# Kernel tuning notes

Measured on AMD Instinct MI355X. Metric: run time of the kernel, lower is better.

## Reference

```python
import jax, jax.numpy as jnp
import numpy as np

SIZE = 14          # feature-map side (448 image / stride 32)
IMG_STRIDE = 32    # feature->image coordinate stride
RATIOS = [(4, 4), (3, 5), (5, 3), (6, 6), (5, 7), (7, 5), (8, 8), (6, 10), (10, 6)]
GROUPS = [(0, 3), (3, 6), (6, 9)]   # ratio index ranges per scale group
N_LIST = [3, 2, 1]                   # proposals kept per group (sum = proposalN = 6)
IOU_THRESHS = [0.25, 0.25, 0.25]
WIN_NUMS = [(SIZE - h + 1) * (SIZE - w + 1) for h, w in RATIOS]  # 121,120,120,81,80,80,49,45,45
OFFS = np.cumsum([0] + WIN_NUMS)


def _make_coords():
    # image-space [x0,y0,x1,y1] per window, same order as flattened avgpool outputs
    coords = []
    for h, w in RATIOS:
        Ho, Wo = SIZE - h + 1, SIZE - w + 1
        for i in range(Ho):
            for j in range(Wo):
                x0 = i * IMG_STRIDE - 1
                y0 = j * IMG_STRIDE - 1
                x1 = x0 + h * IMG_STRIDE
                y1 = y0 + w * IMG_STRIDE
                coords.append([max(x0, 0), max(y0, 0), x1, y1])
    return np.asarray(coords, np.int32)  # [741, 4]


def setup_inputs() -> dict:
    key = jax.random.key(0)
    B = 65536
    x = jax.random.normal(key, (B, 1, SIZE, SIZE), dtype=jnp.float32)
    coords = jnp.asarray(_make_coords())
    return {"x": x, "coords": coords, "proposalN": 6}


def _avgpool_scores(x):
    # x: [B,1,H,W] -> concat of flattened VALID avgpools, [B, sum(WIN_NUMS)]
    B = x.shape[0]
    outs = []
    for h, w in RATIOS:
        s = jax.lax.reduce_window(x, 0.0, jax.lax.add, (1, 1, h, w), (1, 1, 1, 1), 'VALID')
        outs.append((s / (h * w)).reshape(B, -1))
    return jnp.concatenate(outs, axis=1)


def _nms_group(scores, coords_f, areas, N, thresh):
    # greedy NMS: repeatedly take argmax of remaining scores, suppress IoU>thresh.
    # Matches the torch/numpy loop (sorted-walk == repeated argmax for distinct scores).
    W = scores.shape[0]
    def step(carry, _):
        mask, last = carry
        any_v = jnp.any(mask)
        idx = jnp.argmax(jnp.where(mask, scores, -jnp.inf)).astype(jnp.int32)
        idx = jnp.where(any_v, idx, last)  # if exhausted, repeat last pick (as original)
        c = coords_f[idx]
        lx = jnp.minimum(coords_f[:, 2], c[2]) - jnp.maximum(coords_f[:, 0], c[0]) + 1.0
        ly = jnp.minimum(coords_f[:, 3], c[3]) - jnp.maximum(coords_f[:, 1], c[1]) + 1.0
        inter = jnp.where((lx < 0) | (ly < 0), 0.0, lx * ly)
        iou = inter / (areas + areas[idx] - inter)
        return (mask & (iou <= thresh), idx), idx
    init = (jnp.ones((W,), dtype=bool), jnp.int32(0))
    _, idxs = jax.lax.scan(step, init, None, length=N)
    return idxs  # [N] int32


def reference(x, coords, proposalN):
    all_scores = _avgpool_scores(x)                 # [B, 741]
    coords_f = coords.astype(jnp.float32)
    areas = (coords_f[:, 2] - coords_f[:, 0] + 1.0) * (coords_f[:, 3] - coords_f[:, 1] + 1.0)
    idx_parts = []
    for g, (a, b) in enumerate(GROUPS):
        s, e = int(OFFS[a]), int(OFFS[b])
        cf, ar = coords_f[s:e], areas[s:e]
        N, t = N_LIST[g], IOU_THRESHS[g]
        f = lambda sc, cf=cf, ar=ar, N=N, t=t: _nms_group(sc, cf, ar, N, t)
        idx_parts.append(jax.vmap(f)(all_scores[:, s:e]) + s)  # [B, N]
    proposalN_indices = jnp.concatenate(idx_parts, axis=1)      # [B, proposalN]
    proposalN_windows_scores = jnp.take_along_axis(all_scores, proposalN_indices, axis=1)
    window_scores = all_scores
    return proposalN_indices, proposalN_windows_scores, window_scores
```

## Files before the change

### kernel.cpp

```cpp
#include <hip/hip_runtime.h>
#include <stdint.h>

#define NW 741
#define NEG_INF_KEY 0x007FFFFFu

typedef float f2 __attribute__((ext_vector_type(2)));

static __device__ __forceinline__ unsigned score_key(float f) {
  const unsigned u = __float_as_uint(f);
  return (u & 0x80000000u) ? ~u : (u | 0x80000000u);
}
static __device__ __forceinline__ float key_score(unsigned k) {
  return __uint_as_float((k & 0x80000000u) ? (k ^ 0x80000000u) : ~k);
}

template<int CTRL>
static __device__ __forceinline__ unsigned max_step(unsigned m) {
  const unsigned t = (unsigned)__builtin_amdgcn_update_dpp(0, (int)m, CTRL, 0xF, 0xF, true);
  return m > t ? m : t;
}
template<int CTRL>
static __device__ __forceinline__ int min_step(int c) {
  const int t = __builtin_amdgcn_update_dpp(0x7fffffff, c, CTRL, 0xF, 0xF, false);
  return c < t ? c : t;
}
static __device__ __forceinline__ void wave_argmax(unsigned& k, int& i) {
  unsigned m = k;
  m = max_step<0x111>(m);
  m = max_step<0x112>(m);
  m = max_step<0x114>(m);
  m = max_step<0x118>(m);
  m = max_step<0x142>(m);
  m = max_step<0x143>(m);
  const unsigned smax = (unsigned)__builtin_amdgcn_readlane((int)m, 63);
  int ci = (k == smax) ? i : 0x7fffffff;
  ci = min_step<0x111>(ci);
  ci = min_step<0x112>(ci);
  ci = min_step<0x114>(ci);
  ci = min_step<0x118>(ci);
  ci = min_step<0x142>(ci);
  ci = min_step<0x143>(ci);
  k = smax;
  i = __builtin_amdgcn_readlane(ci, 63);
}

struct Rinfo { int off, Wo, h, w; };
constexpr Rinfo RINF[7] = {
  {0, 11, 4, 4}, {121, 10, 3, 5}, {241, 12, 5, 3}, {361, 9, 6, 6},
  {442, 8, 5, 7}, {522, 10, 7, 5}, {602, 7, 8, 8}};
constexpr int findr(int g) {
  int r = 0;
  for (int k = 0; k < 7; ++k) if (g >= RINF[k].off) r = k;
  return r;
}

template<int SB>
static __device__ __forceinline__ void slot_boxar(const int lane, float4& b, float& ar) {
  constexpr int r1 = findr(SB);
  constexpr int r2 = findr(SB + 63);
  const int g = SB + lane;
  int i, j, h, w;
  {
    constexpr Rinfo R = RINF[r1];
    const int o = g - R.off;
    i = o / R.Wo; j = o - i * R.Wo; h = R.h; w = R.w;
  }
  if constexpr (r2 != r1) {
    constexpr Rinfo R = RINF[r2];
    if (g >= R.off) {
      const int o = g - R.off;
      i = o / R.Wo; j = o - i * R.Wo; h = R.h; w = R.w;
    }
  }
  const float x0 = (i > 0) ? (float)(i * 32 - 1) : 0.0f;
  const float y0 = (j > 0) ? (float)(j * 32 - 1) : 0.0f;
  const float x1 = (float)(i * 32 - 1 + h * 32);
  const float y1 = (float)(j * 32 - 1 + w * 32);
  b = make_float4(x0, y0, x1, y1);
  ar = (x1 - x0 + 1.0f) * (y1 - y0 + 1.0f);
}

static __device__ __forceinline__ void box_uniform(const int idx, float4& b, float& a) {
  int i, j, h, w;
  if (idx >= 522)      { const int o = idx - 522; i = o / 10; j = o - i * 10; h = 7; w = 5; }
  else if (idx >= 442) { const int o = idx - 442; i = o / 8;  j = o - i * 8;  h = 5; w = 7; }
  else if (idx >= 361) { const int o = idx - 361; i = o / 9;  j = o - i * 9;  h = 6; w = 6; }
  else if (idx >= 241) { const int o = idx - 241; i = o / 12; j = o - i * 12; h = 5; w = 3; }
  else if (idx >= 121) { const int o = idx - 121; i = o / 10; j = o - i * 10; h = 3; w = 5; }
  else                 { const int o = idx;       i = o / 11; j = o - i * 11; h = 4; w = 4; }
  const float x0 = (i > 0) ? (float)(i * 32 - 1) : 0.0f;
  const float y0 = (j > 0) ? (float)(j * 32 - 1) : 0.0f;
  const float x1 = (float)(i * 32 - 1 + h * 32);
  const float y1 = (float)(j * 32 - 1 + w * 32);
  b = make_float4(x0, y0, x1, y1);
  a = (x1 - x0 + 1.0f) * (y1 - y0 + 1.0f);
}

template<int H, int W, int OFF, int S0>
static __device__ __forceinline__ void slot2(const f2* __restrict__ im2,
                                             float* __restrict__ wrowA,
                                             float* __restrict__ wrowB,
                                             const int lane, const bool hasB,
                                             unsigned& ka, unsigned& kb) {
  constexpr int Wo = 14 - W + 1;
  constexpr int NWIN = (14 - H + 1) * Wo;
  const int o = S0 + lane;
  ka = 0u; kb = 0u;
  if (o < NWIN) {
    const int i = o / Wo, j = o - i * Wo;
    const f2* p = im2 + (i * 14 + j);
    f2 acc = {0.0f, 0.0f};
#pragma unroll
    for (int di = 0; di < H; ++di)
#pragma unroll
      for (int dj = 0; dj < W; ++dj)
        acc += p[di * 14 + dj];
    const float scA = acc.x / (float)(H * W);
    const float scB = acc.y / (float)(H * W);
    wrowA[OFF + o] = scA;
    if (hasB) wrowB[OFF + o] = scB;
    ka = score_key(scA);
    kb = score_key(scB);
  }
}

template<int H, int W, int OFF>
static __device__ __forceinline__ void gslot(const float* __restrict__ img,
                                             float* __restrict__ wrow,
                                             const int lane, unsigned& k) {
  constexpr int Wo = 14 - W + 1;
  constexpr int NWIN = (14 - H + 1) * Wo;
  k = 0u;
  if (lane < NWIN) {
    const int i = lane / Wo, j = lane - i * Wo;
    const float* p = img + i * 14 + j;
    float acc = 0.0f;
#pragma unroll
    for (int di = 0; di < H; ++di)
#pragma unroll
      for (int dj = 0; dj < W; ++dj)
        acc += p[di * 14 + dj];
    const float sc = acc / (float)(H * W);
    wrow[OFF + lane] = sc;
    k = score_key(sc);
  }
}

#define SUP2F(KA, KB, SB) {                                         \
    float4 cb; float ar; slot_boxar<SB>(lane, cb, ar);              \
    float lx = fminf(cb.z, bA.z) - fmaxf(cb.x, bA.x) + 1.0f;        \
    float ly = fminf(cb.w, bA.w) - fmaxf(cb.y, bA.y) + 1.0f;        \
    float in = (lx < 0.0f || ly < 0.0f) ? 0.0f : lx * ly;           \
    if (4.0f * in > ar + aA - in) KA = 0u;                          \
    lx = fminf(cb.z, bB.z) - fmaxf(cb.x, bB.x) + 1.0f;              \
    ly = fminf(cb.w, bB.w) - fmaxf(cb.y, bB.y) + 1.0f;              \
    in = (lx < 0.0f || ly < 0.0f) ? 0.0f : lx * ly;                 \
    if (4.0f * in > ar + aB - in) KB = 0u; }

#define SCAN6(bk, bi, K0, K1, K2, K3, K4, K5, S0, S1, S2, S3, S4, S5) \
    bk = K0; bi = (S0) + lane;                                        \
    if (K1 > bk) { bk = K1; bi = (S1) + lane; }                       \
    if (K2 > bk) { bk = K2; bi = (S2) + lane; }                       \
    if (K3 > bk) { bk = K3; bi = (S3) + lane; }                       \
    if (K4 > bk) { bk = K4; bi = (S4) + lane; }                       \
    if (K5 > bk) { bk = K5; bi = (S5) + lane; }

#define SELPICK(bk, bi, last, lastS, idx, sc)                 \
    if (bk > NEG_INF_KEY) { idx = bi; sc = key_score(bk); }   \
    else { idx = last; sc = lastS; }                          \
    last = idx; lastS = sc;

__global__ __launch_bounds__(256) void appm_kernel(
    const float* __restrict__ x, const int* __restrict__ coords,
    float* __restrict__ out, int B) {

  __shared__ f2 imgp[4][196];
  (void)coords;

  const int t = threadIdx.x;
  const int wv = t >> 6;
  const int lane = t & 63;
  const int img0 = blockIdx.x * 8;
  const int imgA = img0 + wv * 2;
  const int imgB = imgA + 1;
  const bool hasA = (imgA < B);
  const bool hasB = (imgB < B);

  {
    int nimg = B - img0; if (nimg > 8) nimg = 8;
    const float* xb = x + (long long)img0 * 196;
    for (int u = t; u < 784; u += 256) {
      const int pr = u / 196, k = u - pr * 196;
      const int iA = 2 * pr, iB = iA + 1;
      f2 v;
      v.x = (iA < nimg) ? xb[iA * 196 + k] : 0.0f;
      v.y = (iB < nimg) ? xb[iB * 196 + k] : 0.0f;
      imgp[pr][k] = v;
    }
  }
  __syncthreads();

  if (hasA) {
    const f2* im2 = imgp[wv];
    float* wrowA = out + (long long)B * 12 + (long long)imgA * NW;
    float* wrowB = wrowA + NW;

    float myIA = 0.0f, mySA = 0.0f, myIB = 0.0f, mySB = 0.0f;
    unsigned bkA, bkB; int biA, biB;
    int idxA, idxB; float scA, scB;

    {
      unsigned kA0, kA1, kA2, kA3, kA4, kA5, kB0, kB1, kB2, kB3, kB4, kB5;
      slot2<4, 4, 0, 0>(im2, wrowA, wrowB, lane, hasB, kA0, kB0);
      slot2<4, 4, 0, 64>(im2, wrowA, wrowB, lane, hasB, kA1, kB1);
      slot2<3, 5, 121, 0>(im2, wrowA, wrowB, lane, hasB, kA2, kB2);
      slot2<3, 5, 121, 64>(im2, wrowA, wrowB, lane, hasB, kA3, kB3);
      slot2<5, 3, 241, 0>(im2, wrowA, wrowB, lane, hasB, kA4, kB4);
      slot2<5, 3, 241, 64>(im2, wrowA, wrowB, lane, hasB, kA5, kB5);

      int lastA = 0, lastB = 0; float lastSA = 0.0f, lastSB = 0.0f;
      SCAN6(bkA, biA, kA0, kA1, kA2, kA3, kA4, kA5, 0, 64, 121, 185, 241, 305);
      SCAN6(bkB, biB, kB0, kB1, kB2, kB3, kB4, kB5, 0, 64, 121, 185, 241, 305);
      wave_argmax(bkA, biA); wave_argmax(bkB, biB);
      SELPICK(bkA, biA, lastA, lastSA, idxA, scA);
      SELPICK(bkB, biB, lastB, lastSB, idxB, scB);
      if (lane == 0) { myIA = (float)idxA; mySA = scA; myIB = (float)idxB; mySB = scB; }
      {
        float4 bA, bB; float aA, aB;
        box_uniform(idxA, bA, aA); box_uniform(idxB, bB, aB);
        SUP2F(kA0, kB0, 0); SUP2F(kA1, kB1, 64); SUP2F(kA2, kB2, 121);
        SUP2F(kA3, kB3, 185); SUP2F(kA4, kB4, 241); SUP2F(kA5, kB5, 305);
      }
      SCAN6(bkA, biA, kA0, kA1, kA2, kA3, kA4, kA5, 0, 64, 121, 185, 241, 305);
      SCAN6(bkB, biB, kB0, kB1, kB2, kB3, kB4, kB5, 0, 64, 121, 185, 241, 305);
      wave_argmax(bkA, biA); wave_argmax(bkB, biB);
      SELPICK(bkA, biA, lastA, lastSA, idxA, scA);
      SELPICK(bkB, biB, lastB, lastSB, idxB, scB);
      if (lane == 1) { myIA = (float)idxA; mySA = scA; myIB = (float)idxB; mySB = scB; }
      {
        float4 bA, bB; float aA, aB;
        box_uniform(idxA, bA, aA); box_uniform(idxB, bB, aB);
        SUP2F(kA0, kB0, 0); SUP2F(kA1, kB1, 64); SUP2F(kA2, kB2, 121);
        SUP2F(kA3, kB3, 185); SUP2F(kA4, kB4, 241); SUP2F(kA5, kB5, 305);
      }
      SCAN6(bkA, biA, kA0, kA1, kA2, kA3, kA4, kA5, 0, 64, 121, 185, 241, 305);
      SCAN6(bkB, biB, kB0, kB1, kB2, kB3, kB4, kB5, 0, 64, 121, 185, 241, 305);
      wave_argmax(bkA, biA); wave_argmax(bkB, biB);
      SELPICK(bkA, biA, lastA, lastSA, idxA, scA);
      SELPICK(bkB, biB, lastB, lastSB, idxB, scB);
      if (lane == 2) { myIA = (float)idxA; mySA = scA; myIB = (float)idxB; mySB = scB; }
    }

    {
      unsigned kA6, kA7, kA8, kA9, kA10, kA11, kB6, kB7, kB8, kB9, kB10, kB11;
      slot2<6, 6, 361, 0>(im2, wrowA, wrowB, lane, hasB, kA6, kB6);
      slot2<6, 6, 361, 64>(im2, wrowA, wrowB, lane, hasB, kA7, kB7);
      slot2<5, 7, 442, 0>(im2, wrowA, wrowB, lane, hasB, kA8, kB8);
      slot2<5, 7, 442, 64>(im2, wrowA, wrowB, lane, hasB, kA9, kB9);
      slot2<7, 5, 522, 0>(im2, wrowA, wrowB, lane, hasB, kA10, kB10);
      slot2<7, 5, 522, 64>(im2, wrowA, wrowB, lane, hasB, kA11, kB11);

      int lastA = 361, lastB = 361; float lastSA = 0.0f, lastSB = 0.0f;
      SCAN6(bkA, biA, kA6, kA7, kA8, kA9, kA10, kA11, 361, 425, 442, 506, 522, 586);
      SCAN6(bkB, biB, kB6, kB7, kB8, kB9, kB10, kB11, 361, 425, 442, 506, 522, 586);
      wave_argmax(bkA, biA); wave_argmax(bkB, biB);
      SELPICK(bkA, biA, lastA, lastSA, idxA, scA);
      SELPICK(bkB, biB, lastB, lastSB, idxB, scB);
      if (lane == 3) { myIA = (float)idxA; mySA = scA; myIB = (float)idxB; mySB = scB; }
      {
        float4 bA, bB; float aA, aB;
        box_uniform(idxA, bA, aA); box_uniform(idxB, bB, aB);
        SUP2F(kA6, kB6, 361); SUP2F(kA7, kB7, 425); SUP2F(kA8, kB8, 442);
        SUP2F(kA9, kB9, 506); SUP2F(kA10, kB10, 522); SUP2F(kA11, kB11, 586);
      }
      SCAN6(bkA, biA, kA6, kA7, kA8, kA9, kA10, kA11, 361, 425, 442, 506, 522, 586);
      SCAN6(bkB, biB, kB6, kB7, kB8, kB9, kB10, kB11, 361, 425, 442, 506, 522, 586);
      wave_argmax(bkA, biA); wave_argmax(bkB, biB);
      SELPICK(bkA, biA, lastA, lastSA, idxA, scA);
      SELPICK(bkB, biB, lastB, lastSB, idxB, scB);
      if (lane == 4) { myIA = (float)idxA; mySA = scA; myIB = (float)idxB; mySB = scB; }
    }

    {
      const float* xA = x + (long long)imgA * 196;
      unsigned tA, tB;
      unsigned gkA, gkB; int giA, giB;
      gslot<8, 8, 602>(xA, wrowA, lane, tA);
      gkA = tA; giA = 602 + lane;
      gslot<6, 10, 651>(xA, wrowA, lane, tA);
      if (tA > gkA) { gkA = tA; giA = 651 + lane; }
      gslot<10, 6, 696>(xA, wrowA, lane, tA);
      if (tA > gkA) { gkA = tA; giA = 696 + lane; }

      gkB = 0u; giB = 602 + lane;
      if (hasB) {
        const float* xB = x + (long long)imgB * 196;
        gslot<8, 8, 602>(xB, wrowB, lane, tB);
        gkB = tB;
        gslot<6, 10, 651>(xB, wrowB, lane, tB);
        if (tB > gkB) { gkB = tB; giB = 651 + lane; }
        gslot<10, 6, 696>(xB, wrowB, lane, tB);
        if (tB > gkB) { gkB = tB; giB = 696 + lane; }
      }

      wave_argmax(gkA, giA); wave_argmax(gkB, giB);
      if (gkA > NEG_INF_KEY) { idxA = giA; scA = key_score(gkA); }
      else { idxA = 602; scA = 0.0f; }
      if (gkB > NEG_INF_KEY) { idxB = giB; scB = key_score(gkB); }
      else { idxB = 602; scB = 0.0f; }
      if (lane == 5) { myIA = (float)idxA; mySA = scA; myIB = (float)idxB; mySB = scB; }
    }

    if (lane < 6) {
      const long long a6 = (long long)imgA * 6 + lane;
      out[a6] = myIA;
      out[(long long)B * 6 + a6] = mySA;
      if (hasB) {
        const long long b6 = (long long)imgB * 6 + lane;
        out[b6] = myIB;
        out[(long long)B * 6 + b6] = mySB;
      }
    }
  }
}

extern "C" void kernel_launch(void* const* d_in, const int* in_sizes, int n_in,
                              void* d_out, int out_size, void* d_ws, size_t ws_size,
                              hipStream_t stream) {
  const float* x = (const float*)d_in[0];
  const int* coords = (const int*)d_in[1];
  float* out = (float*)d_out;
  const int B = in_sizes[0] / 196;
  const int nblk = (B + 7) / 8;
  appm_kernel<<<dim3(nblk), dim3(256), 0, stream>>>(x, coords, out, B);
}
```

Baseline: 379.5 us.

## Process four images per wavefront with float4-interleaved shared memory

Each wavefront now handles four images instead of two. Their pixels are interleaved as float4 in LDS, so one LDS load feeds four accumulators, and the box and IoU setup plus the wave reductions are amortised over more images. The last scale group now reads from the shared tile rather than from global memory. Blocks cover 16 images, which means more registers per thread, possibly lower occupancy, and more strided scalar writes into the interleaved LDS layout.

```diff
diff --git a/kernel.cpp b/kernel.cpp
--- a/kernel.cpp
+++ b/kernel.cpp
@@ -4,7 +4,7 @@
 #define NW 741
 #define NEG_INF_KEY 0x007FFFFFu
 
-typedef float f2 __attribute__((ext_vector_type(2)));
+typedef float f4 __attribute__((ext_vector_type(4)));
 
 static __device__ __forceinline__ unsigned score_key(float f) {
   const unsigned u = __float_as_uint(f);
@@ -97,65 +97,39 @@
 }
 
 template<int H, int W, int OFF, int S0>
-static __device__ __forceinline__ void slot2(const f2* __restrict__ im2,
-                                             float* __restrict__ wrowA,
-                                             float* __restrict__ wrowB,
-                                             const int lane, const bool hasB,
-                                             unsigned& ka, unsigned& kb) {
+static __device__ __forceinline__ void slot4(const f4* __restrict__ im4,
+                                             float* __restrict__ wr0,
+                                             float* __restrict__ wr1,
+                                             float* __restrict__ wr2,
+                                             float* __restrict__ wr3,
+                                             const int lane,
+                                             const bool h1, const bool h2, const bool h3,
+                                             unsigned& k0, unsigned& k1,
+                                             unsigned& k2, unsigned& k3) {
   constexpr int Wo = 14 - W + 1;
   constexpr int NWIN = (14 - H + 1) * Wo;
   const int o = S0 + lane;
-  ka = 0u; kb = 0u;
+  k0 = 0u; k1 = 0u; k2 = 0u; k3 = 0u;
   if (o < NWIN) {
     const int i = o / Wo, j = o - i * Wo;
-    const f2* p = im2 + (i * 14 + j);
-    f2 acc = {0.0f, 0.0f};
+    const f4* p = im4 + (i * 14 + j);
+    f4 acc = {0.0f, 0.0f, 0.0f, 0.0f};
 #pragma unroll
     for (int di = 0; di < H; ++di)
 #pragma unroll
       for (int dj = 0; dj < W; ++dj)
         acc += p[di * 14 + dj];
-    const float scA = acc.x / (float)(H * W);
-    const float scB = acc.y / (float)(H * W);
-    wrowA[OFF + o] = scA;
-    if (hasB) wrowB[OFF + o] = scB;
-    ka = score_key(scA);
-    kb = score_key(scB);
-  }
-}
-
-template<int H, int W, int OFF>
-static __device__ __forceinline__ void gslot(const float* __restrict__ img,
-                                             float* __restrict__ wrow,
-                                             const int lane, unsigned& k) {
-  constexpr int Wo = 14 - W + 1;
-  constexpr int NWIN = (14 - H + 1) * Wo;
-  k = 0u;
-  if (lane < NWIN) {
-    const int i = lane / Wo, j = lane - i * Wo;
-    const float* p = img + i * 14 + j;
-    float acc = 0.0f;
-#pragma unroll
-    for (int di = 0; di < H; ++di)
-#pragma unroll
-      for (int dj = 0; dj < W; ++dj)
-        acc += p[di * 14 + dj];
-    const float sc = acc / (float)(H * W);
-    wrow[OFF + lane] = sc;
-    k = score_key(sc);
-  }
-}
-
-#define SUP2F(KA, KB, SB) {                                         \
-    float4 cb; float ar; slot_boxar<SB>(lane, cb, ar);              \
-    float lx = fminf(cb.z, bA.z) - fmaxf(cb.x, bA.x) + 1.0f;        \
-    float ly = fminf(cb.w, bA.w) - fmaxf(cb.y, bA.y) + 1.0f;        \
-    float in = (lx < 0.0f || ly < 0.0f) ? 0.0f : lx * ly;           \
-    if (4.0f * in > ar + aA - in) KA = 0u;                          \
-    lx = fminf(cb.z, bB.z) - fmaxf(cb.x, bB.x) + 1.0f;              \
-    ly = fminf(cb.w, bB.w) - fmaxf(cb.y, bB.y) + 1.0f;              \
-    in = (lx < 0.0f || ly < 0.0f) ? 0.0f : lx * ly;                 \
-    if (4.0f * in > ar + aB - in) KB = 0u; }
+    const float s0 = acc.x / (float)(H * W);
+    const float s1 = acc.y / (float)(H * W);
+    const float s2 = acc.z / (float)(H * W);
+    const float s3 = acc.w / (float)(H * W);
+    wr0[OFF + o] = s0;
+    if (h1) wr1[OFF + o] = s1;
+    if (h2) wr2[OFF + o] = s2;
+    if (h3) wr3[OFF + o] = s3;
+    k0 = score_key(s0); k1 = score_key(s1); k2 = score_key(s2); k3 = score_key(s3);
+  }
+}
 
 #define SCAN6(bk, bi, K0, K1, K2, K3, K4, K5, S0, S1, S2, S3, S4, S5) \
     bk = K0; bi = (S0) + lane;                                        \
@@ -165,161 +139,177 @@
     if (K4 > bk) { bk = K4; bi = (S4) + lane; }                       \
     if (K5 > bk) { bk = K5; bi = (S5) + lane; }
 
-#define SELPICK(bk, bi, last, lastS, idx, sc)                 \
-    if (bk > NEG_INF_KEY) { idx = bi; sc = key_score(bk); }   \
-    else { idx = last; sc = lastS; }                          \
-    last = idx; lastS = sc;
+#define GSCAN(c, A0, A1, A2, A3, A4, A5) \
+    SCAN6(bk##c, bi##c, q##c##0, q##c##1, q##c##2, q##c##3, q##c##4, q##c##5, \
+          A0, A1, A2, A3, A4, A5)
+
+#define ARGMAX4 \
+    wave_argmax(bk0, bi0); wave_argmax(bk1, bi1); \
+    wave_argmax(bk2, bi2); wave_argmax(bk3, bi3);
+
+#define SELPICK4(c)                                                   \
+    if (bk##c > NEG_INF_KEY) { idx##c = bi##c; sc##c = key_score(bk##c); } \
+    else { idx##c = last##c; sc##c = lastS##c; }                      \
+    last##c = idx##c; lastS##c = sc##c;
+
+#define SELPICK_ALL SELPICK4(0) SELPICK4(1) SELPICK4(2) SELPICK4(3)
+
+#define STORE_PICK(PL) if (lane == (PL)) {                  \
+    myI0 = (float)idx0; myS0 = sc0; myI1 = (float)idx1; myS1 = sc1; \
+    myI2 = (float)idx2; myS2 = sc2; myI3 = (float)idx3; myS3 = sc3; }
+
+#define BOXES4 \
+    float4 b0, b1, b2, b3; float a0, a1, a2, a3;  \
+    box_uniform(idx0, b0, a0); box_uniform(idx1, b1, a1); \
+    box_uniform(idx2, b2, a2); box_uniform(idx3, b3, a3);
+
+#define SUPIOU(BC, AC, K) {                                        \
+    float lx = fminf(cb.z, BC.z) - fmaxf(cb.x, BC.x) + 1.0f;       \
+    float ly = fminf(cb.w, BC.w) - fmaxf(cb.y, BC.y) + 1.0f;       \
+    float in = (lx < 0.0f || ly < 0.0f) ? 0.0f : lx * ly;          \
+    if (4.0f * in > ar + AC - in) K = 0u; }
+#define SUPSLOT(SB, K0, K1, K2, K3) {                              \
+    float4 cb; float ar; slot_boxar<SB>(lane, cb, ar);             \
+    SUPIOU(b0, a0, K0) SUPIOU(b1, a1, K1)                          \
+    SUPIOU(b2, a2, K2) SUPIOU(b3, a3, K3) }
 
 __global__ __launch_bounds__(256) void appm_kernel(
     const float* __restrict__ x, const int* __restrict__ coords,
     float* __restrict__ out, int B) {
 
-  __shared__ f2 imgp[4][196];
+  __shared__ f4 imgp[4][196];
   (void)coords;
 
   const int t = threadIdx.x;
   const int wv = t >> 6;
   const int lane = t & 63;
-  const int img0 = blockIdx.x * 8;
-  const int imgA = img0 + wv * 2;
-  const int imgB = imgA + 1;
-  const bool hasA = (imgA < B);
-  const bool hasB = (imgB < B);
+  const int img0 = blockIdx.x * 16;
+  const int imgA = img0 + wv * 4;
+  const bool has0 = (imgA < B);
+  const bool h1 = (imgA + 1 < B);
+  const bool h2 = (imgA + 2 < B);
+  const bool h3 = (imgA + 3 < B);
 
   {
-    int nimg = B - img0; if (nimg > 8) nimg = 8;
+    int nimg = B - img0; if (nimg > 16) nimg = 16;
     const float* xb = x + (long long)img0 * 196;
-    for (int u = t; u < 784; u += 256) {
-      const int pr = u / 196, k = u - pr * 196;
-      const int iA = 2 * pr, iB = iA + 1;
-      f2 v;
-      v.x = (iA < nimg) ? xb[iA * 196 + k] : 0.0f;
-      v.y = (iB < nimg) ? xb[iB * 196 + k] : 0.0f;
-      imgp[pr][k] = v;
+    for (int u = t; u < 3136; u += 256) {
+      const int i = u / 196, k = u - i * 196;
+      const float v = (i < nimg) ? xb[i * 196 + k] : 0.0f;
+      ((float*)&imgp[i >> 2][k])[i & 3] = v;
     }
   }
   __syncthreads();
 
-  if (hasA) {
-    const f2* im2 = imgp[wv];
-    float* wrowA = out + (long long)B * 12 + (long long)imgA * NW;
-    float* wrowB = wrowA + NW;
-
-    float myIA = 0.0f, mySA = 0.0f, myIB = 0.0f, mySB = 0.0f;
-    unsigned bkA, bkB; int biA, biB;
-    int idxA, idxB; float scA, scB;
+  if (has0) {
+    const f4* im4 = imgp[wv];
+    float* wr0 = out + (long long)B * 12 + (long long)imgA * NW;
+    float* wr1 = wr0 + NW;
+    float* wr2 = wr0 + 2 * NW;
+    float* wr3 = wr0 + 3 * NW;
+
+    float myI0 = 0.0f, myS0 = 0.0f, myI1 = 0.0f, myS1 = 0.0f;
+    float myI2 = 0.0f, myS2 = 0.0f, myI3 = 0.0f, myS3 = 0.0f;
+    unsigned bk0, bk1, bk2, bk3; int bi0, bi1, bi2, bi3;
+    int idx0, idx1, idx2, idx3; float sc0, sc1, sc2, sc3;
 
     {
-      unsigned kA0, kA1, kA2, kA3, kA4, kA5, kB0, kB1, kB2, kB3, kB4, kB5;
-      slot2<4, 4, 0, 0>(im2, wrowA, wrowB, lane, hasB, kA0, kB0);
-      slot2<4, 4, 0, 64>(im2, wrowA, wrowB, lane, hasB, kA1, kB1);
-      slot2<3, 5, 121, 0>(im2, wrowA, wrowB, lane, hasB, kA2, kB2);
-      slot2<3, 5, 121, 64>(im2, wrowA, wrowB, lane, hasB, kA3, kB3);
-      slot2<5, 3, 241, 0>(im2, wrowA, wrowB, lane, hasB, kA4, kB4);
-      slot2<5, 3, 241, 64>(im2, wrowA, wrowB, lane, hasB, kA5, kB5);
-
-      int lastA = 0, lastB = 0; float lastSA = 0.0f, lastSB = 0.0f;
-      SCAN6(bkA, biA, kA0, kA1, kA2, kA3, kA4, kA5, 0, 64, 121, 185, 241, 305);
-      SCAN6(bkB, biB, kB0, kB1, kB2, kB3, kB4, kB5, 0, 64, 121, 185, 241, 305);
-      wave_argmax(bkA, biA); wave_argmax(bkB, biB);
-      SELPICK(bkA, biA, lastA, lastSA, idxA, scA);
-      SELPICK(bkB, biB, lastB, lastSB, idxB, scB);
-      if (lane == 0) { myIA = (float)idxA; mySA = scA; myIB = (float)idxB; mySB = scB; }
+      unsigned q00, q01, q02, q03, q04, q05;
+      unsigned q10, q11, q12, q13, q14, q15;
+      unsigned q20, q21, q22, q23, q24, q25;
+      unsigned q30, q31, q32, q33, q34, q35;
+      slot4<4, 4, 0, 0>(im4, wr0, wr1, wr2, wr3, lane, h1, h2, h3, q00, q10, q20, q30);
+      slot4<4, 4, 0, 64>(im4, wr0, wr1, wr2, wr3, lane, h1, h2, h3, q01, q11, q21, q31);
+      slot4<3, 5, 121, 0>(im4, wr0, wr1, wr2, wr3, lane, h1, h2, h3, q02, q12, q22, q32);
+      slot4<3, 5, 121, 64>(im4, wr0, wr1, wr2, wr3, lane, h1, h2, h3, q03, q13, q23, q33);
+      slot4<5, 3, 241, 0>(im4, wr0, wr1, wr2, wr3, lane, h1, h2, h3, q04, q14, q24, q34);
+      slot4<5, 3, 241, 64>(im4, wr0, wr1, wr2, wr3, lane, h1, h2, h3, q05, q15, q25, q35);
+
+      int last0 = 0, last1 = 0, last2 = 0, last3 = 0;
+      float lastS0 = 0.0f, lastS1 = 0.0f, lastS2 = 0.0f, lastS3 = 0.0f;
+      GSCAN(0, 0, 64, 121, 185, 241, 305); GSCAN(1, 0, 64, 121, 185, 241, 305);
+      GSCAN(2, 0, 64, 121, 185, 241, 305); GSCAN(3, 0, 64, 121, 185, 241, 305);
+      ARGMAX4; SELPICK_ALL; STORE_PICK(0);
       {
-        float4 bA, bB; float aA, aB;
-        box_uniform(idxA, bA, aA); box_uniform(idxB, bB, aB);
-        SUP2F(kA0, kB0, 0); SUP2F(kA1, kB1, 64); SUP2F(kA2, kB2, 121);
-        SUP2F(kA3, kB3, 185); SUP2F(kA4, kB4, 241); SUP2F(kA5, kB5, 305);
+        BOXES4;
+        SUPSLOT(0, q00, q10, q20, q30); SUPSLOT(64, q01, q11, q21, q31);
+        SUPSLOT(121, q02, q12, q22, q32); SUPSLOT(185, q03, q13, q23, q33);
+        SUPSLOT(241, q04, q14, q24, q34); SUPSLOT(305, q05, q15, q25, q35);
       }
-      SCAN6(bkA, biA, kA0, kA1, kA2, kA3, kA4, kA5, 0, 64, 121, 185, 241, 305);
-      SCAN6(bkB, biB, kB0, kB1, kB2, kB3, kB4, kB5, 0, 64, 121, 185, 241, 305);
-      wave_argmax(bkA, biA); wave_argmax(bkB, biB);
-      SELPICK(bkA, biA, lastA, lastSA, idxA, scA);
-      SELPICK(bkB, biB, lastB, lastSB, idxB, scB);
-      if (lane == 1) { myIA = (float)idxA; mySA = scA; myIB = (float)idxB; mySB = scB; }
+      GSCAN(0, 0, 64, 121, 185, 241, 305); GSCAN(1, 0, 64, 121, 185, 241, 305);
+      GSCAN(2, 0, 64, 121, 185, 241, 305); GSCAN(3, 0, 64, 121, 185, 241, 305);
+      ARGMAX4; SELPICK_ALL; STORE_PICK(1);
       {
-        float4 bA, bB; float aA, aB;
-        box_uniform(idxA, bA, aA); box_uniform(idxB, bB, aB);
-        SUP2F(kA0, kB0, 0); SUP2F(kA1, kB1, 64); SUP2F(kA2, kB2, 121);
-        SUP2F(kA3, kB3, 185); SUP2F(kA4, kB4, 241); SUP2F(kA5, kB5, 305);
+        BOXES4;
+        SUPSLOT(0, q00, q10, q20, q30); SUPSLOT(64, q01, q11, q21, q31);
+        SUPSLOT(121, q02, q12, q22, q32); SUPSLOT(185, q03, q13, q23, q33);
+        SUPSLOT(241, q04, q14, q24, q34); SUPSLOT(305, q05, q15, q25, q35);
       }
-      SCAN6(bkA, biA, kA0, kA1, kA2, kA3, kA4, kA5, 0, 64, 121, 185, 241, 305);
-      SCAN6(bkB, biB, kB0, kB1, kB2, kB3, kB4, kB5, 0, 64, 121, 185, 241, 305);
-      wave_argmax(bkA, biA); wave_argmax(bkB, biB);
-      SELPICK(bkA, biA, lastA, lastSA, idxA, scA);
-      SELPICK(bkB, biB, lastB, lastSB, idxB, scB);
-      if (lane == 2) { myIA = (float)idxA; mySA = scA; myIB = (float)idxB; mySB = scB; }
+      GSCAN(0, 0, 64, 121, 185, 241, 305); GSCAN(1, 0, 64, 121, 185, 241, 305);
+      GSCAN(2, 0, 64, 121, 185, 241, 305); GSCAN(3, 0, 64, 121, 185, 241, 305);
+      ARGMAX4; SELPICK_ALL; STORE_PICK(2);
     }
 
     {
-      unsigned kA6, kA7, kA8, kA9, kA10, kA11, kB6, kB7, kB8, kB9, kB10, kB11;
-      slot2<6, 6, 361, 0>(im2, wrowA, wrowB, lane, hasB, kA6, kB6);
-      slot2<6, 6, 361, 64>(im2, wrowA, wrowB, lane, hasB, kA7, kB7);
-      slot2<5, 7, 442, 0>(im2, wrowA, wrowB, lane, hasB, kA8, kB8);
-      slot2<5, 7, 442, 64>(im2, wrowA, wrowB, lane, hasB, kA9, kB9);
-      slot2<7, 5, 522, 0>(im2, wrowA, wrowB, lane, hasB, kA10, kB10);
-      slot2<7, 5, 522, 64>(im2, wrowA, wrowB, lane, hasB, kA11, kB11);
-
-      int lastA = 361, lastB = 361; float lastSA = 0.0f, lastSB = 0.0f;
-      SCAN6(bkA, biA, kA6, kA7, kA8, kA9, kA10, kA11, 361, 425, 442, 506, 522, 586);
-      SCAN6(bkB, biB, kB6, kB7, kB8, kB9, kB10, kB11, 361, 425, 442, 506, 522, 586);
-      wave_argmax(bkA, biA); wave_argmax(bkB, biB);
-      SELPICK(bkA, biA, lastA, lastSA, idxA, scA);
-      SELPICK(bkB, biB, lastB, lastSB, idxB, scB);
-      if (lane == 3) { myIA = (float)idxA; mySA = scA; myIB = (float)idxB; mySB = scB; }
+      unsigned q00, q01, q02, q03, q04, q05;
+      unsigned q10, q11, q12, q13, q14, q15;
+      unsigned q20, q21, q22, q23, q24, q25;
+      unsigned q30, q31, q32, q33, q34, q35;
+      slot4<6, 6, 361, 0>(im4, wr0, wr1, wr2, wr3, lane, h1, h2, h3, q00, q10, q20, q30);
+      slot4<6, 6, 361, 64>(im4, wr0, wr1, wr2, wr3, lane, h1, h2, h3, q01, q11, q21, q31);
+      slot4<5, 7, 442, 0>(im4, wr0, wr1, wr2, wr3, lane, h1, h2, h3, q02, q12, q22, q32);
+      slot4<5, 7, 442, 64>(im4, wr0, wr1, wr2, wr3, lane, h1, h2, h3, q03, q13, q23, q33);
+      slot4<7, 5, 522, 0>(im4, wr0, wr1, wr2, wr3, lane, h1, h2, h3, q04, q14, q24, q34);
+      slot4<7, 5, 522, 64>(im4, wr0, wr1, wr2, wr3, lane, h1, h2, h3, q05, q15, q25, q35);
+
+      int last0 = 361, last1 = 361, last2 = 361, last3 = 361;
+      float lastS0 = 0.0f, lastS1 = 0.0f, lastS2 = 0.0f, lastS3 = 0.0f;
+      GSCAN(0, 361, 425, 442, 506, 522, 586); GSCAN(1, 361, 425, 442, 506, 522, 586);
+      GSCAN(2, 361, 425, 442, 506, 522, 586); GSCAN(3, 361, 425, 442, 506, 522, 586);
+      ARGMAX4; SELPICK_ALL; STORE_PICK(3);
       {
-        float4 bA, bB; float aA, aB;
-        box_uniform(idxA, bA, aA); box_uniform(idxB, bB, aB);
-        SUP2F(kA6, kB6, 361); SUP2F(kA7, kB7, 425); SUP2F(kA8, kB8, 442);
-        SUP2F(kA9, kB9, 506); SUP2F(kA10, kB10, 522); SUP2F(kA11, kB11, 586);
+        BOXES4;
+        SUPSLOT(361, q00, q10, q20, q30); SUPSLOT(425, q01, q11, q21, q31);
+        SUPSLOT(442, q02, q12, q22, q32); SUPSLOT(506, q03, q13, q23, q33);
+        SUPSLOT(522, q04, q14, q24, q34); SUPSLOT(586, q05, q15, q25, q35);
       }
-      SCAN6(bkA, biA, kA6, kA7, kA8, kA9, kA10, kA11, 361, 425, 442, 506, 522, 586);
-      SCAN6(bkB, biB, kB6, kB7, kB8, kB9, kB10, kB11, 361, 425, 442, 506, 522, 586);
-      wave_argmax(bkA, biA); wave_argmax(bkB, biB);
-      SELPICK(bkA, biA, lastA, lastSA, idxA, scA);
-      SELPICK(bkB, biB, lastB, lastSB, idxB, scB);
-      if (lane == 4) { myIA = (float)idxA; mySA = scA; myIB = (float)idxB; mySB = scB; }
+      GSCAN(0, 361, 425, 442, 506, 522, 586); GSCAN(1, 361, 425, 442, 506, 522, 586);
+      GSCAN(2, 361, 425, 442, 506, 522, 586); GSCAN(3, 361, 425, 442, 506, 522, 586);
+      ARGMAX4; SELPICK_ALL; STORE_PICK(4);
     }
 
     {
-      const float* xA = x + (long long)imgA * 196;
-      unsigned tA, tB;
-      unsigned gkA, gkB; int giA, giB;
-      gslot<8, 8, 602>(xA, wrowA, lane, tA);
-      gkA = tA; giA = 602 + lane;
-      gslot<6, 10, 651>(xA, wrowA, lane, tA);
-      if (tA > gkA) { gkA = tA; giA = 651 + lane; }
-      gslot<10, 6, 696>(xA, wrowA, lane, tA);
-      if (tA > gkA) { gkA = tA; giA = 696 + lane; }
-
-      gkB = 0u; giB = 602 + lane;
-      if (hasB) {
-        const float* xB = x + (long long)imgB * 196;
-        gslot<8, 8, 602>(xB, wrowB, lane, tB);
-        gkB = tB;
-        gslot<6, 10, 651>(xB, wrowB, lane, tB);
-        if (tB > gkB) { gkB = tB; giB = 651 + lane; }
-        gslot<10, 6, 696>(xB, wrowB, lane, tB);
-        if (tB > gkB) { gkB = tB; giB = 696 + lane; }
-      }
-
-      wave_argmax(gkA, giA); wave_argmax(gkB, giB);
-      if (gkA > NEG_INF_KEY) { idxA = giA; scA = key_score(gkA); }
-      else { idxA = 602; scA = 0.0f; }
-      if (gkB > NEG_INF_KEY) { idxB = giB; scB = key_score(gkB); }
-      else { idxB = 602; scB = 0.0f; }
-      if (lane == 5) { myIA = (float)idxA; mySA = scA; myIB = (float)idxB; mySB = scB; }
+      unsigned t0, t1, t2, t3;
+      slot4<8, 8, 602, 0>(im4, wr0, wr1, wr2, wr3, lane, h1, h2, h3, t0, t1, t2, t3);
+      unsigned gk0 = t0, gk1 = t1, gk2 = t2, gk3 = t3;
+      int gi0 = 602 + lane, gi1 = 602 + lane, gi2 = 602 + lane, gi3 = 602 + lane;
+      slot4<6, 10, 651, 0>(im4, wr0, wr1, wr2, wr3, lane, h1, h2, h3, t0, t1, t2, t3);
+      if (t0 > gk0) { gk0 = t0; gi0 = 651 + lane; }
+      if (t1 > gk1) { gk1 = t1; gi1 = 651 + lane; }
+      if (t2 > gk2) { gk2 = t2; gi2 = 651 + lane; }
+      if (t3 > gk3) { gk3 = t3; gi3 = 651 + lane; }
+      slot4<10, 6, 696, 0>(im4, wr0, wr1, wr2, wr3, lane, h1, h2, h3, t0, t1, t2, t3);
+      if (t0 > gk0) { gk0 = t0; gi0 = 696 + lane; }
+      if (t1 > gk1) { gk1 = t1; gi1 = 696 + lane; }
+      if (t2 > gk2) { gk2 = t2; gi2 = 696 + lane; }
+      if (t3 > gk3) { gk3 = t3; gi3 = 696 + lane; }
+
+      wave_argmax(gk0, gi0); wave_argmax(gk1, gi1);
+      wave_argmax(gk2, gi2); wave_argmax(gk3, gi3);
+      if (gk0 > NEG_INF_KEY) { idx0 = gi0; sc0 = key_score(gk0); } else { idx0 = 602; sc0 = 0.0f; }
+      if (gk1 > NEG_INF_KEY) { idx1 = gi1; sc1 = key_score(gk1); } else { idx1 = 602; sc1 = 0.0f; }
+      if (gk2 > NEG_INF_KEY) { idx2 = gi2; sc2 = key_score(gk2); } else { idx2 = 602; sc2 = 0.0f; }
+      if (gk3 > NEG_INF_KEY) { idx3 = gi3; sc3 = key_score(gk3); } else { idx3 = 602; sc3 = 0.0f; }
+      STORE_PICK(5);
     }
 
     if (lane < 6) {
-      const long long a6 = (long long)imgA * 6 + lane;
-      out[a6] = myIA;
-      out[(long long)B * 6 + a6] = mySA;
-      if (hasB) {
-        const long long b6 = (long long)imgB * 6 + lane;
-        out[b6] = myIB;
-        out[(long long)B * 6 + b6] = mySB;
-      }
+      const long long base = (long long)imgA * 6 + lane;
+      const long long sb = (long long)B * 6;
+      out[base] = myI0;          out[sb + base] = myS0;
+      if (h1) { out[base + 6] = myI1;  out[sb + base + 6] = myS1; }
+      if (h2) { out[base + 12] = myI2; out[sb + base + 12] = myS2; }
+      if (h3) { out[base + 18] = myI3; out[sb + base + 18] = myS3; }
     }
   }
 }
@@ -331,6 +321,6 @@
   const int* coords = (const int*)d_in[1];
   float* out = (float*)d_out;
   const int B = in_sizes[0] / 196;
-  const int nblk = (B + 7) / 8;
+  const int nblk = (B + 15) / 16;
   appm_kernel<<<dim3(nblk), dim3(256), 0, stream>>>(x, coords, out, B);
 }
```

Measured after the change: 367.2 us. 3.3% less time.
